# Kernel optimization log

Measured on AMD Instinct MI355X. Metric: run time of the kernel, lower is better.

## Reference

```python
import jax, jax.numpy as jnp
import numpy as np

B, POOL, PACK = 4096, 45, 15
E, D, V = 512, 8, 30000  # embedding_dim, internal_dims, num_cards
SQRT_D = float(np.sqrt(D))


def setup_inputs() -> dict:
    key = jax.random.key(0)
    ks = jax.random.split(key, 12)
    s = 0.02
    return {
        "pool": jax.random.randint(ks[0], (B, POOL), 0, V),
        "pack": jax.random.randint(ks[1], (B, PACK), 0, V),
        "wins": jax.random.uniform(ks[2], (B,), dtype=jnp.float32),
        "ranks": jax.random.uniform(ks[3], (B,), dtype=jnp.float32),
        "emb_table": jax.random.normal(ks[4], (V, E), dtype=jnp.float32) * s,
        "win_w": jax.random.normal(ks[5], (E, 1), dtype=jnp.float32) * s,
        "win_b": jnp.zeros((E,), dtype=jnp.float32),
        "rank_w": jax.random.normal(ks[6], (E, 1), dtype=jnp.float32) * s,
        "rank_b": jnp.zeros((E,), dtype=jnp.float32),
        "q_w": jax.random.normal(ks[7], (D, E), dtype=jnp.float32) * s,
        "k_w": jax.random.normal(ks[8], (D, E), dtype=jnp.float32) * s,
        "v_w": jax.random.normal(ks[9], (D, E), dtype=jnp.float32) * s,
        "sc_w": jax.random.normal(ks[10], (1, D), dtype=jnp.float32) * s,
        "sc_b": jnp.zeros((1,), dtype=jnp.float32),
    }


def reference(pool, pack, wins, ranks, emb_table, win_w, win_b,
              rank_w, rank_b, q_w, k_w, v_w, sc_w, sc_b):
    pool_emb = emb_table[pool]                                   # [B, POOL, E]
    pack_emb = emb_table[pack]                                   # [B, PACK, E]
    win_emb = wins[:, None, None] * win_w[:, 0] + win_b          # [B, 1, E]
    rank_emb = ranks[:, None, None] * rank_w[:, 0] + rank_b      # [B, 1, E]
    pool_full = jnp.concatenate([pool_emb, win_emb, rank_emb], axis=1)  # [B, POOL+2, E]
    pool_full = jax.nn.relu(pool_full)
    q = jnp.einsum("bke,de->bkd", pack_emb, q_w)                 # [B, PACK, D]
    k = jnp.einsum("bpe,de->bpd", pool_full, k_w)                # [B, POOL+2, D]
    v = jnp.einsum("bpe,de->bpd", pool_full, v_w)                # [B, POOL+2, D]
    scores = jnp.einsum("bkd,bpd->bkp", q, k) / SQRT_D
    attn = jax.nn.softmax(jax.nn.relu(scores), axis=-1)          # [B, PACK, POOL+2]
    context = jnp.einsum("bkp,bpd->bkd", attn, v)                # [B, PACK, D]
    context = jax.nn.leaky_relu(context, negative_slope=0.01)
    logits = jnp.einsum("bkd,od->bko", context, sc_w) + sc_b     # [B, PACK, 1]
    return logits[..., 0]                                        # [B, PACK]
```

## Files before the change

### kernel.cpp

```cpp
#include <hip/hip_runtime.h>

#define B_N 4096
#define POOL_N 45
#define PACK_N 15
#define E_N 512
#define D_N 8
#define V_N 30000

#define WT_SZ  (E_N * 24)
#define TAB_SZ (V_N * 24)

__global__ __launch_bounds__(256) void k_transpose_w(const float* __restrict__ q_w,
                                                     const float* __restrict__ k_w,
                                                     const float* __restrict__ v_w,
                                                     float* __restrict__ wt) {
  int i = blockIdx.x * 256 + threadIdx.x;
  if (i >= E_N * 24) return;
  int e = i / 24, j = i % 24;
  float val = (j < 8) ? q_w[j * E_N + e]
            : (j < 16) ? k_w[(j - 8) * E_N + e]
                       : v_w[(j - 16) * E_N + e];
  wt[i] = val;
}

__global__ __launch_bounds__(512) void k_build_tab(const float* __restrict__ emb,
                                                   const float* __restrict__ wt,
                                                   float* __restrict__ tab) {
  __shared__ float red[8][64][25];
  int lane = threadIdx.x & 63;
  int w = __builtin_amdgcn_readfirstlane(threadIdx.x >> 6);
  int r = blockIdx.x * 64 + lane;
  float acc[24];
#pragma unroll
  for (int j = 0; j < 24; ++j) acc[j] = 0.f;
  if (r < V_N) {
    const float* a = emb + (size_t)r * E_N + w * 64;
    const float* wp = wt + (w * 64) * 24;
#pragma unroll 4
    for (int i = 0; i < 16; ++i) {
      float4 av = ((const float4*)a)[i];
      float xs[4] = {av.x, av.y, av.z, av.w};
#pragma unroll
      for (int c = 0; c < 4; ++c) {
        float x = xs[c];
        float xr = fmaxf(x, 0.f);
        const float* wr = wp + (i * 4 + c) * 24;
#pragma unroll
        for (int j = 0; j < 8; ++j) acc[j] = fmaf(x, wr[j], acc[j]);
#pragma unroll
        for (int j = 8; j < 24; ++j) acc[j] = fmaf(xr, wr[j], acc[j]);
      }
    }
  }
#pragma unroll
  for (int j = 0; j < 24; ++j) red[w][lane][j] = acc[j];
  __syncthreads();
  int t = threadIdx.x;
#pragma unroll
  for (int i = 0; i < 3; ++i) {
    int o = t + 512 * i;
    int row = o / 24, col = o - row * 24;
    int r_out = blockIdx.x * 64 + row;
    if (r_out < V_N) {
      float v = 0.f;
#pragma unroll
      for (int s = 0; s < 8; ++s) v += red[s][row][col];
      tab[(size_t)r_out * 24 + col] = v;
    }
  }
}

__global__ __launch_bounds__(512) void k_build_aux(const float* __restrict__ wins,
                                                   const float* __restrict__ ranks,
                                                   const float* __restrict__ win_w,
                                                   const float* __restrict__ win_b,
                                                   const float* __restrict__ rank_w,
                                                   const float* __restrict__ rank_b,
                                                   const float* __restrict__ wt,
                                                   float* __restrict__ aux) {
  __shared__ float red[8][64][16];
  int lane = threadIdx.x;
  int seg = __builtin_amdgcn_readfirstlane(threadIdx.y);
  int which = blockIdx.y;
  int b = blockIdx.x * 64 + lane;
  float s = which ? ranks[b] : wins[b];
  const float* ww = which ? rank_w : win_w;
  const float* wb = which ? rank_b : win_b;
  float acc[16];
#pragma unroll
  for (int j = 0; j < 16; ++j) acc[j] = 0.f;
  int e0 = seg * 64;
  for (int e = e0; e < e0 + 64; ++e) {
    float x = fmaf(s, ww[e], wb[e]);
    float xr = fmaxf(x, 0.f);
    const float* wr = wt + e * 24 + 8;
#pragma unroll
    for (int j = 0; j < 16; ++j) acc[j] = fmaf(xr, wr[j], acc[j]);
  }
#pragma unroll
  for (int j = 0; j < 16; ++j) red[seg][lane][j] = acc[j];
  __syncthreads();
  int t = threadIdx.x + 64 * threadIdx.y;
#pragma unroll
  for (int rep = 0; rep < 2; ++rep) {
    int o = t + rep * 512;
    int bi = o >> 4, j = o & 15;
    float v = 0.f;
#pragma unroll
    for (int sgi = 0; sgi < 8; ++sgi) v += red[sgi][bi][j];
    aux[(size_t)(blockIdx.x * 64 + bi) * 32 + which * 16 + j] = v;
  }
}

__global__ __launch_bounds__(256) void k_main(const int* __restrict__ pool,
                                              const int* __restrict__ pack,
                                              const float* __restrict__ tab,
                                              const float* __restrict__ aux,
                                              const float* __restrict__ sc_w,
                                              const float* __restrict__ sc_b,
                                              float* __restrict__ out) {
  int grp = threadIdx.x >> 5;
  int lane = threadIdx.x & 31;
  int b = blockIdx.x * 8 + grp;
  int k = (lane < PACK_N) ? lane : 0;
  int qidx = pack[(size_t)b * PACK_N + k];
  const float* qr = tab + (size_t)qidx * 24;
  float4 qa = *(const float4*)qr;
  float4 qb = *(const float4*)(qr + 4);
  const float rs = 0.35355339059327373f;
  const float* auxb = aux + (size_t)b * 32;
  float s[47];
  float m = 0.f;
#pragma unroll
  for (int p = 0; p < 47; ++p) {
    const float* kr;
    if (p < POOL_N) {
      int pi = pool[(size_t)b * POOL_N + p];
      kr = tab + (size_t)pi * 24 + 8;
    } else if (p == POOL_N) {
      kr = auxb;
    } else {
      kr = auxb + 16;
    }
    float4 ka = *(const float4*)kr;
    float4 kb4 = *(const float4*)(kr + 4);
    float d = qa.x * ka.x;
    d = fmaf(qa.y, ka.y, d);
    d = fmaf(qa.z, ka.z, d);
    d = fmaf(qa.w, ka.w, d);
    d = fmaf(qb.x, kb4.x, d);
    d = fmaf(qb.y, kb4.y, d);
    d = fmaf(qb.z, kb4.z, d);
    d = fmaf(qb.w, kb4.w, d);
    d = fmaxf(d * rs, 0.f);
    s[p] = d;
    m = fmaxf(m, d);
  }
  float sum = 0.f;
#pragma unroll
  for (int p = 0; p < 47; ++p) {
    float e = __expf(s[p] - m);
    s[p] = e;
    sum += e;
  }
  float ctx[8] = {0.f, 0.f, 0.f, 0.f, 0.f, 0.f, 0.f, 0.f};
#pragma unroll
  for (int p = 0; p < 47; ++p) {
    const float* vr;
    if (p < POOL_N) {
      int pi = pool[(size_t)b * POOL_N + p];
      vr = tab + (size_t)pi * 24 + 16;
    } else if (p == POOL_N) {
      vr = auxb + 8;
    } else {
      vr = auxb + 24;
    }
    float4 va = *(const float4*)vr;
    float4 vb4 = *(const float4*)(vr + 4);
    float w = s[p];
    ctx[0] = fmaf(w, va.x, ctx[0]);
    ctx[1] = fmaf(w, va.y, ctx[1]);
    ctx[2] = fmaf(w, va.z, ctx[2]);
    ctx[3] = fmaf(w, va.w, ctx[3]);
    ctx[4] = fmaf(w, vb4.x, ctx[4]);
    ctx[5] = fmaf(w, vb4.y, ctx[5]);
    ctx[6] = fmaf(w, vb4.z, ctx[6]);
    ctx[7] = fmaf(w, vb4.w, ctx[7]);
  }
  float inv = 1.f / sum;
  float logit = 0.f;
#pragma unroll
  for (int d0 = 0; d0 < 8; ++d0) {
    float c = ctx[d0] * inv;
    c = (c > 0.f) ? c : 0.01f * c;
    logit = fmaf(c, sc_w[d0], logit);
  }
  logit += sc_b[0];
  if (lane < PACK_N) out[(size_t)b * PACK_N + lane] = logit;
}

extern "C" void kernel_launch(void* const* d_in, const int* in_sizes, int n_in,
                              void* d_out, int out_size, void* d_ws, size_t ws_size,
                              hipStream_t stream) {
  const int* pool = (const int*)d_in[0];
  const int* pack = (const int*)d_in[1];
  const float* wins = (const float*)d_in[2];
  const float* ranks = (const float*)d_in[3];
  const float* emb = (const float*)d_in[4];
  const float* win_w = (const float*)d_in[5];
  const float* win_b = (const float*)d_in[6];
  const float* rank_w = (const float*)d_in[7];
  const float* rank_b = (const float*)d_in[8];
  const float* q_w = (const float*)d_in[9];
  const float* k_w = (const float*)d_in[10];
  const float* v_w = (const float*)d_in[11];
  const float* sc_w = (const float*)d_in[12];
  const float* sc_b = (const float*)d_in[13];

  float* ws = (float*)d_ws;
  float* wt = ws;
  float* tab = ws + WT_SZ;
  float* aux = ws + WT_SZ + TAB_SZ;
  float* out = (float*)d_out;

  hipLaunchKernelGGL(k_transpose_w, dim3(48), dim3(256), 0, stream,
                     q_w, k_w, v_w, wt);
  hipLaunchKernelGGL(k_build_tab, dim3((V_N + 63) / 64), dim3(512), 0, stream,
                     emb, wt, tab);
  hipLaunchKernelGGL(k_build_aux, dim3(B_N / 64, 2), dim3(64, 8), 0, stream,
                     wins, ranks, win_w, win_b, rank_w, rank_b, wt, aux);
  hipLaunchKernelGGL(k_main, dim3(B_N / 8), dim3(256), 0, stream,
                     pool, pack, tab, aux, sc_w, sc_b, out);
}
```

Baseline: 61.55 us.

## Fuse attention into single-pass online softmax and retile aux kernel

```diff
diff --git a/kernel.cpp b/kernel.cpp
--- a/kernel.cpp
+++ b/kernel.cpp
@@ -70,7 +70,7 @@
   }
 }
 
-__global__ __launch_bounds__(512) void k_build_aux(const float* __restrict__ wins,
+__global__ __launch_bounds__(256) void k_build_aux(const float* __restrict__ wins,
                                                    const float* __restrict__ ranks,
                                                    const float* __restrict__ win_w,
                                                    const float* __restrict__ win_b,
@@ -78,19 +78,20 @@
                                                    const float* __restrict__ rank_b,
                                                    const float* __restrict__ wt,
                                                    float* __restrict__ aux) {
-  __shared__ float red[8][64][16];
-  int lane = threadIdx.x;
-  int seg = __builtin_amdgcn_readfirstlane(threadIdx.y);
+  __shared__ float red[16][16][17];
+  int t = threadIdx.x;
+  int bl = t & 15, seg = t >> 4;
   int which = blockIdx.y;
-  int b = blockIdx.x * 64 + lane;
+  int b = blockIdx.x * 16 + bl;
   float s = which ? ranks[b] : wins[b];
   const float* ww = which ? rank_w : win_w;
   const float* wb = which ? rank_b : win_b;
   float acc[16];
 #pragma unroll
   for (int j = 0; j < 16; ++j) acc[j] = 0.f;
-  int e0 = seg * 64;
-  for (int e = e0; e < e0 + 64; ++e) {
+  int e0 = seg * 32;
+#pragma unroll 4
+  for (int e = e0; e < e0 + 32; ++e) {
     float x = fmaf(s, ww[e], wb[e]);
     float xr = fmaxf(x, 0.f);
     const float* wr = wt + e * 24 + 8;
@@ -98,18 +99,13 @@
     for (int j = 0; j < 16; ++j) acc[j] = fmaf(xr, wr[j], acc[j]);
   }
 #pragma unroll
-  for (int j = 0; j < 16; ++j) red[seg][lane][j] = acc[j];
+  for (int j = 0; j < 16; ++j) red[seg][bl][j] = acc[j];
   __syncthreads();
-  int t = threadIdx.x + 64 * threadIdx.y;
-#pragma unroll
-  for (int rep = 0; rep < 2; ++rep) {
-    int o = t + rep * 512;
-    int bi = o >> 4, j = o & 15;
-    float v = 0.f;
-#pragma unroll
-    for (int sgi = 0; sgi < 8; ++sgi) v += red[sgi][bi][j];
-    aux[(size_t)(blockIdx.x * 64 + bi) * 32 + which * 16 + j] = v;
-  }
+  int bi = t >> 4, j = t & 15;
+  float v = 0.f;
+#pragma unroll
+  for (int sg = 0; sg < 16; ++sg) v += red[sg][bi][j];
+  aux[(size_t)(blockIdx.x * 16 + bi) * 32 + which * 16 + j] = v;
 }
 
 __global__ __launch_bounds__(256) void k_main(const int* __restrict__ pool,
@@ -122,6 +118,8 @@
   int grp = threadIdx.x >> 5;
   int lane = threadIdx.x & 31;
   int b = blockIdx.x * 8 + grp;
+  int i0 = pool[(size_t)b * POOL_N + lane];
+  int i1 = (lane < POOL_N - 32) ? pool[(size_t)b * POOL_N + 32 + lane] : 0;
   int k = (lane < PACK_N) ? lane : 0;
   int qidx = pack[(size_t)b * PACK_N + k];
   const float* qr = tab + (size_t)qidx * 24;
@@ -129,64 +127,53 @@
   float4 qb = *(const float4*)(qr + 4);
   const float rs = 0.35355339059327373f;
   const float* auxb = aux + (size_t)b * 32;
-  float s[47];
-  float m = 0.f;
-#pragma unroll
-  for (int p = 0; p < 47; ++p) {
-    const float* kr;
-    if (p < POOL_N) {
-      int pi = pool[(size_t)b * POOL_N + p];
-      kr = tab + (size_t)pi * 24 + 8;
-    } else if (p == POOL_N) {
-      kr = auxb;
-    } else {
-      kr = auxb + 16;
-    }
-    float4 ka = *(const float4*)kr;
-    float4 kb4 = *(const float4*)(kr + 4);
-    float d = qa.x * ka.x;
-    d = fmaf(qa.y, ka.y, d);
-    d = fmaf(qa.z, ka.z, d);
-    d = fmaf(qa.w, ka.w, d);
-    d = fmaf(qb.x, kb4.x, d);
-    d = fmaf(qb.y, kb4.y, d);
-    d = fmaf(qb.z, kb4.z, d);
-    d = fmaf(qb.w, kb4.w, d);
+
+  float m = 0.f, sum = 0.f;
+  float ctx[8] = {0.f, 0.f, 0.f, 0.f, 0.f, 0.f, 0.f, 0.f};
+
+  auto att_step = [&](const float* kr) {
+    float4 k0 = *(const float4*)kr;
+    float4 k1 = *(const float4*)(kr + 4);
+    float4 v0 = *(const float4*)(kr + 8);
+    float4 v1 = *(const float4*)(kr + 12);
+    float d = qa.x * k0.x;
+    d = fmaf(qa.y, k0.y, d);
+    d = fmaf(qa.z, k0.z, d);
+    d = fmaf(qa.w, k0.w, d);
+    d = fmaf(qb.x, k1.x, d);
+    d = fmaf(qb.y, k1.y, d);
+    d = fmaf(qb.z, k1.z, d);
+    d = fmaf(qb.w, k1.w, d);
     d = fmaxf(d * rs, 0.f);
-    s[p] = d;
+    float t = __expf(-fabsf(d - m));
+    bool up = d > m;
+    float sc = up ? t : 1.f;
+    float e = up ? 1.f : t;
     m = fmaxf(m, d);
-  }
-  float sum = 0.f;
-#pragma unroll
-  for (int p = 0; p < 47; ++p) {
-    float e = __expf(s[p] - m);
-    s[p] = e;
-    sum += e;
-  }
-  float ctx[8] = {0.f, 0.f, 0.f, 0.f, 0.f, 0.f, 0.f, 0.f};
-#pragma unroll
-  for (int p = 0; p < 47; ++p) {
-    const float* vr;
-    if (p < POOL_N) {
-      int pi = pool[(size_t)b * POOL_N + p];
-      vr = tab + (size_t)pi * 24 + 16;
-    } else if (p == POOL_N) {
-      vr = auxb + 8;
-    } else {
-      vr = auxb + 24;
-    }
-    float4 va = *(const float4*)vr;
-    float4 vb4 = *(const float4*)(vr + 4);
-    float w = s[p];
-    ctx[0] = fmaf(w, va.x, ctx[0]);
-    ctx[1] = fmaf(w, va.y, ctx[1]);
-    ctx[2] = fmaf(w, va.z, ctx[2]);
-    ctx[3] = fmaf(w, va.w, ctx[3]);
-    ctx[4] = fmaf(w, vb4.x, ctx[4]);
-    ctx[5] = fmaf(w, vb4.y, ctx[5]);
-    ctx[6] = fmaf(w, vb4.z, ctx[6]);
-    ctx[7] = fmaf(w, vb4.w, ctx[7]);
-  }
+    sum = fmaf(sum, sc, e);
+    ctx[0] = fmaf(ctx[0], sc, e * v0.x);
+    ctx[1] = fmaf(ctx[1], sc, e * v0.y);
+    ctx[2] = fmaf(ctx[2], sc, e * v0.z);
+    ctx[3] = fmaf(ctx[3], sc, e * v0.w);
+    ctx[4] = fmaf(ctx[4], sc, e * v1.x);
+    ctx[5] = fmaf(ctx[5], sc, e * v1.y);
+    ctx[6] = fmaf(ctx[6], sc, e * v1.z);
+    ctx[7] = fmaf(ctx[7], sc, e * v1.w);
+  };
+
+#pragma unroll 8
+  for (int p = 0; p < 32; ++p) {
+    int pi = __shfl(i0, p, 32);
+    att_step(tab + (size_t)pi * 24 + 8);
+  }
+#pragma unroll
+  for (int p = 0; p < 13; ++p) {
+    int pi = __shfl(i1, p, 32);
+    att_step(tab + (size_t)pi * 24 + 8);
+  }
+  att_step(auxb);
+  att_step(auxb + 16);
+
   float inv = 1.f / sum;
   float logit = 0.f;
 #pragma unroll
@@ -227,7 +214,7 @@
                      q_w, k_w, v_w, wt);
   hipLaunchKernelGGL(k_build_tab, dim3((V_N + 63) / 64), dim3(512), 0, stream,
                      emb, wt, tab);
-  hipLaunchKernelGGL(k_build_aux, dim3(B_N / 64, 2), dim3(64, 8), 0, stream,
+  hipLaunchKernelGGL(k_build_aux, dim3(B_N / 16, 2), dim3(256), 0, stream,
                      wins, ranks, win_w, win_b, rank_w, rank_b, wt, aux);
   hipLaunchKernelGGL(k_main, dim3(B_N / 8), dim3(256), 0, stream,
                      pool, pack, tab, aux, sc_w, sc_b, out);
```

New measurement: 53.83 us. -12.5%, faster.
